# Performance work log

Hardware: AMD Instinct MI355X
Metric: run time of the kernel (lower is better)

Reference implementation:

```python
import jax, jax.numpy as jnp
import numpy as np

N_HEAD = 16
MASK_VALUE = -10000.0


def setup_inputs() -> dict:
    key = jax.random.key(0)
    ks = jax.random.split(key, 5)
    B, S, D = 2, 2048, 1024
    return {
        "x": jax.random.normal(ks[0], (B, S, D), dtype=jnp.float32),
        "qkv_w": jax.random.normal(ks[1], (D, 3 * D), dtype=jnp.float32) * 0.02,
        "qkv_b": jnp.zeros((3 * D,), dtype=jnp.float32),
        "proj_w": jax.random.normal(ks[2], (D, D), dtype=jnp.float32) * 0.02,
        "proj_b": jnp.zeros((D,), dtype=jnp.float32),
    }


def reference(x, qkv_w, qkv_b, proj_w, proj_b):
    B, S, D = x.shape
    H = N_HEAD
    hd = D // H

    # fused QKV projection, then split (torch.split along last dim)
    qkv = x @ qkv_w + qkv_b                      # [B, S, 3D]
    q, k, v = jnp.split(qkv, 3, axis=-1)

    def split_heads(t):  # [B, S, D] -> [B, H, S, hd]
        return t.reshape(B, S, H, hd).transpose(0, 2, 1, 3)

    q, k, v = split_heads(q), split_heads(k), split_heads(v)

    # scaled dot-product scores (scale_attn_weights=True)
    scores = jnp.einsum("bhqd,bhkd->bhqk", q, k) / jnp.sqrt(jnp.asarray(hd, x.dtype))

    # causal mask: tril over [query_len, key_len] (no cache, so q_len == k_len == S)
    causal = jnp.tril(jnp.ones((S, S), dtype=bool))[None, None]
    scores = jnp.where(causal, scores, jnp.asarray(MASK_VALUE, x.dtype))

    attn = jax.nn.softmax(scores, axis=-1)       # dropout p=0 (eval): identity
    out = jnp.einsum("bhqk,bhkd->bhqd", attn, v)

    # merge heads and output projection (resid dropout p=0)
    out = out.transpose(0, 2, 1, 3).reshape(B, S, D)
    out = out @ proj_w + proj_b
    return out
```

## Files before the change

kernel.cpp:

```cpp
#include <hip/hip_runtime.h>
#include <hip/hip_bf16.h>


#define SEQ 2048
#define DM 1024
#define HD 64
#define NHEAD 16
#define BHTOT 32

typedef unsigned short u16;
typedef __bf16 bf16_t;
typedef bf16_t bf16x8 __attribute__((ext_vector_type(8)));
typedef float f32x4 __attribute__((ext_vector_type(4)));
typedef float f32x16 __attribute__((ext_vector_type(16)));

__device__ __forceinline__ u16 f2bf(float f) {
  unsigned u = __float_as_uint(f);
  u += 0x7fffu + ((u >> 16) & 1u);
  return (u16)(u >> 16);
}

__device__ __forceinline__ f32x4 mfma16(uint4 a, uint4 b, f32x4 c) {
  return __builtin_amdgcn_mfma_f32_16x16x32_bf16(
      __builtin_bit_cast(bf16x8, a), __builtin_bit_cast(bf16x8, b), c, 0, 0, 0);
}

__device__ __forceinline__ f32x16 mfma32(uint4 a, uint4 b, f32x16 c) {
  return __builtin_amdgcn_mfma_f32_32x32x16_bf16(
      __builtin_bit_cast(bf16x8, a), __builtin_bit_cast(bf16x8, b), c, 0, 0, 0);
}

__device__ __forceinline__ unsigned cvtpk(float lo, float hi) {
  unsigned d;
  asm("v_cvt_pk_bf16_f32 %0, %1, %2" : "=v"(d) : "v"(lo), "v"(hi));
  return d;
}

__device__ __forceinline__ void gload_lds16(const u16* g, void* l) {
  __builtin_amdgcn_global_load_lds(
      (const __attribute__((address_space(1))) unsigned*)g,
      (__attribute__((address_space(3))) unsigned*)l, 16, 0, 0);
}

__global__ __launch_bounds__(256) void cvt_bf16(const float* __restrict__ in,
                                                u16* __restrict__ out) {
  int i = (blockIdx.x * 256 + threadIdx.x) * 4;
  float4 v = *(const float4*)(in + i);
  uint2 pk;
  pk.x = (unsigned)f2bf(v.x) | ((unsigned)f2bf(v.y) << 16);
  pk.y = (unsigned)f2bf(v.z) | ((unsigned)f2bf(v.w) << 16);
  *(uint2*)(out + i) = pk;
}

__global__ __launch_bounds__(256) void transpose_w(const float* __restrict__ W,
                                                   u16* __restrict__ Wt,
                                                   int K, int N) {
  __shared__ u16 t[32][33];
  const int n0 = blockIdx.x * 32, k0 = blockIdx.y * 32;
  const int tx = threadIdx.x & 31, ty = threadIdx.x >> 5;
#pragma unroll
  for (int i = 0; i < 4; ++i) {
    int k = ty + i * 8;
    t[tx][k] = f2bf(W[(size_t)(k0 + k) * N + n0 + tx]);
  }
  __syncthreads();
#pragma unroll
  for (int i = 0; i < 4; ++i) {
    int n = ty + i * 8;
    Wt[(size_t)(n0 + n) * K + k0 + tx] = t[n][tx];
  }
}

__global__ __launch_bounds__(256) void qkv_gemm(
    const u16* __restrict__ A, const u16* __restrict__ Bt,
    const float* __restrict__ bias,
    u16* __restrict__ qb, u16* __restrict__ kb, u16* __restrict__ vb) {
  __shared__ u16 Al[128 * 32];
  __shared__ u16 Bl[128 * 32];
  const int tid = threadIdx.x;
  const int m0 = blockIdx.y * 128;
  const int n0 = blockIdx.x * 128;
  const int w = tid >> 6, lane = tid & 63;
  const int lr = lane & 15, lg = lane >> 4;
  const int wm = (w >> 1) * 64, wn = (w & 1) * 64;
  const int Kd = DM;

  f32x4 acc[4][4] = {};

  for (int kk = 0; kk < Kd; kk += 32) {
    __syncthreads();
#pragma unroll
    for (int i = 0; i < 2; ++i) {
      int off = (i * 4 + w) * 1024 + lane * 16;
      int row = off >> 6, colb = off & 63;
      gload_lds16(A + (size_t)(m0 + row) * Kd + kk + (colb >> 1),
                  (char*)Al + (i * 4 + w) * 1024);
      gload_lds16(Bt + (size_t)(n0 + row) * Kd + kk + (colb >> 1),
                  (char*)Bl + (i * 4 + w) * 1024);
    }
    __syncthreads();
    uint4 af[4], bfr[4];
#pragma unroll
    for (int mi = 0; mi < 4; ++mi)
      af[mi] = *(const uint4*)(Al + (wm + mi * 16 + lr) * 32 + lg * 8);
#pragma unroll
    for (int ni = 0; ni < 4; ++ni)
      bfr[ni] = *(const uint4*)(Bl + (wn + ni * 16 + lr) * 32 + lg * 8);
#pragma unroll
    for (int mi = 0; mi < 4; ++mi)
#pragma unroll
      for (int ni = 0; ni < 4; ++ni)
        acc[mi][ni] = mfma16(af[mi], bfr[ni], acc[mi][ni]);
  }

#pragma unroll
  for (int mi = 0; mi < 4; ++mi) {
#pragma unroll
    for (int ni = 0; ni < 4; ++ni) {
#pragma unroll
      for (int r = 0; r < 4; ++r) {
        int m = m0 + wm + mi * 16 + lg * 4 + r;
        int n = n0 + wn + ni * 16 + lr;
        float v = acc[mi][ni][r] + bias[n];
        int part = n >> 10;
        int d = n & 1023;
        int h = d >> 6, dim = d & 63;
        int b = m >> 11, s = m & 2047;
        int bh = b * NHEAD + h;
        if (part == 0)
          qb[((size_t)bh * SEQ + s) * HD + dim] = f2bf(v * 0.18033688f);
        else if (part == 1)
          kb[((size_t)bh * SEQ + s) * HD + dim] = f2bf(v);
        else
          vb[((size_t)bh * HD + dim) * SEQ + s] = f2bf(v);
      }
    }
  }
}

__global__ __launch_bounds__(128) void attn_kernel(
    const u16* __restrict__ Q, const u16* __restrict__ K,
    const u16* __restrict__ Vt, u16* __restrict__ O) {
  const int lane = threadIdx.x & 63;
  const int w = threadIdx.x >> 6;
  const int r31 = lane & 31;
  const int hi = lane >> 5;
  const int bh = blockIdx.x & 31;
  const int j = 31 - (blockIdx.x >> 5);
  const int qt = 2 * j + w;
  const int q0w = qt * 32;
  const int nst = j + 1;

  const u16* Qb = Q + (size_t)bh * SEQ * HD;
  const u16* Kb = K + (size_t)bh * SEQ * HD;
  const u16* Vb = Vt + (size_t)bh * HD * SEQ;

  uint4 qf[4];
#pragma unroll
  for (int ks = 0; ks < 4; ++ks)
    qf[ks] = *(const uint4*)(Qb + (size_t)(q0w + r31) * HD + ks * 16 + hi * 8);

  f32x16 ot0 = {}, ot1 = {};
  float L = 0.f;

#define LOADK(KF, kv0)                                                          \
  {                                                                             \
    _Pragma("unroll") for (int ks = 0; ks < 4; ++ks) {                          \
      KF[ks] = *(const uint4*)(Kb + (size_t)((kv0) + r31) * HD + ks * 16 + hi * 8); \
      KF[ks + 4] =                                                              \
          *(const uint4*)(Kb + (size_t)((kv0) + 32 + r31) * HD + ks * 16 + hi * 8); \
    }                                                                           \
  }

#define RELAYOUT(dst, S, base)                                                  \
  {                                                                             \
    unsigned e01 = cvtpk(S[base + 0], S[base + 1]), e23 = cvtpk(S[base + 2], S[base + 3]); \
    unsigned e45 = cvtpk(S[base + 4], S[base + 5]), e67 = cvtpk(S[base + 6], S[base + 7]); \
    unsigned p01 = __shfl_xor(e01, 32), p23 = __shfl_xor(e23, 32);              \
    unsigned p45 = __shfl_xor(e45, 32), p67 = __shfl_xor(e67, 32);              \
    dst.x = hi ? p45 : e01;                                                     \
    dst.y = hi ? p67 : e23;                                                     \
    dst.z = hi ? e45 : p01;                                                     \
    dst.w = hi ? e67 : p23;                                                     \
  }

#define STEP(KF, KN)                                                            \
  {                                                                             \
    const int kv0 = t << 6;                                                     \
    const bool last = (t == nst - 1);                                           \
    const bool skip1 = last && ((qt & 1) == 0);   \
    uint4 vf[8];                                                                \
    _Pragma("unroll") for (int ks = 0; ks < 2; ++ks) {                          \
      vf[ks] = *(const uint4*)(Vb + (size_t)r31 * SEQ + kv0 + ks * 16 + hi * 8); \
      vf[ks + 4] =                                                              \
          *(const uint4*)(Vb + (size_t)(32 + r31) * SEQ + kv0 + ks * 16 + hi * 8); \
    }                                                                           \
    if (!skip1) {                                                               \
      _Pragma("unroll") for (int ks = 2; ks < 4; ++ks) {                        \
        vf[ks] = *(const uint4*)(Vb + (size_t)r31 * SEQ + kv0 + ks * 16 + hi * 8); \
        vf[ks + 4] =                                                            \
            *(const uint4*)(Vb + (size_t)(32 + r31) * SEQ + kv0 + ks * 16 + hi * 8); \
      }                                                                         \
    }                                                                           \
    f32x16 s0 = {}, s1 = {};                                                    \
    _Pragma("unroll") for (int ks = 0; ks < 4; ++ks)                            \
        s0 = mfma32(KF[ks], qf[ks], s0);                                        \
    if (!skip1) {                                                               \
      _Pragma("unroll") for (int ks = 0; ks < 4; ++ks)                          \
          s1 = mfma32(KF[ks + 4], qf[ks], s1);                                  \
    }                                                                           \
    if (t + 1 < nst) LOADK(KN, kv0 + 64);                                       \
    if (last) {                                                                 \
      _Pragma("unroll") for (int i = 0; i < 16; ++i) {                          \
        const int row = (i & 3) + 8 * (i >> 2) + 4 * hi;                        \
        if (skip1) {                                                            \
          if (row > r31) s0[i] = -1e30f;                                        \
        } else {                                                                \
          if (row > r31) s1[i] = -1e30f;                                        \
        }                                                                       \
      }                                                                         \
    }                                                                           \
    float rs = 0.f;                                                             \
    _Pragma("unroll") for (int i = 0; i < 16; ++i) {                            \
      s0[i] = __builtin_exp2f(s0[i]);                                           \
      rs += s0[i];                                                              \
    }                                                                           \
    if (!skip1) {                                                               \
      _Pragma("unroll") for (int i = 0; i < 16; ++i) {                          \
        s1[i] = __builtin_exp2f(s1[i]);                                         \
        rs += s1[i];                                                            \
      }                                                                         \
    }                                                                           \
    L += rs;                                                                    \
    uint4 pa[4];                                                                \
    RELAYOUT(pa[0], s0, 0);                                                     \
    RELAYOUT(pa[1], s0, 8);                                                     \
    if (!skip1) {                                                               \
      RELAYOUT(pa[2], s1, 0);                                                   \
      RELAYOUT(pa[3], s1, 8);                                                   \
    }                                                                           \
    _Pragma("unroll") for (int ks = 0; ks < 2; ++ks) {                          \
      ot0 = mfma32(vf[ks], pa[ks], ot0);                                        \
      ot1 = mfma32(vf[ks + 4], pa[ks], ot1);                                    \
    }                                                                           \
    if (!skip1) {                                                               \
      _Pragma("unroll") for (int ks = 2; ks < 4; ++ks) {                        \
        ot0 = mfma32(vf[ks], pa[ks], ot0);                                      \
        ot1 = mfma32(vf[ks + 4], pa[ks], ot1);                                  \
      }                                                                         \
    }                                                                           \
  }

  uint4 kA[8], kB[8];
  LOADK(kA, 0);
  int t = 0;
  for (;;) {
    STEP(kA, kB);
    if (++t >= nst) break;
    STEP(kB, kA);
    if (++t >= nst) break;
  }
#undef STEP
#undef RELAYOUT
#undef LOADK

  L += __shfl_xor(L, 32);
  const float inv = 1.0f / L;
  const int b = bh >> 4, h = bh & 15;
  u16* Orow = O + ((size_t)b * SEQ + q0w + r31) * DM + h * HD;
#pragma unroll
  for (int g = 0; g < 4; ++g) {
    uint2 p0, p1;
    p0.x = (unsigned)f2bf(ot0[4 * g + 0] * inv) | ((unsigned)f2bf(ot0[4 * g + 1] * inv) << 16);
    p0.y = (unsigned)f2bf(ot0[4 * g + 2] * inv) | ((unsigned)f2bf(ot0[4 * g + 3] * inv) << 16);
    p1.x = (unsigned)f2bf(ot1[4 * g + 0] * inv) | ((unsigned)f2bf(ot1[4 * g + 1] * inv) << 16);
    p1.y = (unsigned)f2bf(ot1[4 * g + 2] * inv) | ((unsigned)f2bf(ot1[4 * g + 3] * inv) << 16);
    *(uint2*)(Orow + 8 * g + 4 * hi) = p0;
    *(uint2*)(Orow + 32 + 8 * g + 4 * hi) = p1;
  }
}

__global__ __launch_bounds__(256) void proj_gemm(
    const u16* __restrict__ A, const u16* __restrict__ Bt,
    const float* __restrict__ bias, float* __restrict__ out) {
  __shared__ u16 Al[128 * 32];
  __shared__ u16 Bl[128 * 32];
  const int tid = threadIdx.x;
  const int m0 = blockIdx.y * 128;
  const int n0 = blockIdx.x * 128;
  const int w = tid >> 6, lane = tid & 63;
  const int lr = lane & 15, lg = lane >> 4;
  const int wm = (w >> 1) * 64, wn = (w & 1) * 64;
  const int Kd = DM;

  f32x4 acc[4][4] = {};

  for (int kk = 0; kk < Kd; kk += 32) {
    __syncthreads();
#pragma unroll
    for (int i = 0; i < 2; ++i) {
      int off = (i * 4 + w) * 1024 + lane * 16;
      int row = off >> 6, colb = off & 63;
      gload_lds16(A + (size_t)(m0 + row) * Kd + kk + (colb >> 1),
                  (char*)Al + (i * 4 + w) * 1024);
      gload_lds16(Bt + (size_t)(n0 + row) * Kd + kk + (colb >> 1),
                  (char*)Bl + (i * 4 + w) * 1024);
    }
    __syncthreads();
    uint4 af[4], bfr[4];
#pragma unroll
    for (int mi = 0; mi < 4; ++mi)
      af[mi] = *(const uint4*)(Al + (wm + mi * 16 + lr) * 32 + lg * 8);
#pragma unroll
    for (int ni = 0; ni < 4; ++ni)
      bfr[ni] = *(const uint4*)(Bl + (wn + ni * 16 + lr) * 32 + lg * 8);
#pragma unroll
    for (int mi = 0; mi < 4; ++mi)
#pragma unroll
      for (int ni = 0; ni < 4; ++ni)
        acc[mi][ni] = mfma16(af[mi], bfr[ni], acc[mi][ni]);
  }

#pragma unroll
  for (int mi = 0; mi < 4; ++mi)
#pragma unroll
    for (int ni = 0; ni < 4; ++ni)
#pragma unroll
      for (int r = 0; r < 4; ++r) {
        int m = m0 + wm + mi * 16 + lg * 4 + r;
        int n = n0 + wn + ni * 16 + lr;
        out[(size_t)m * DM + n] = acc[mi][ni][r] + bias[n];
      }
}

extern "C" void kernel_launch(void* const* d_in, const int* in_sizes, int n_in,
                              void* d_out, int out_size, void* d_ws, size_t ws_size,
                              hipStream_t stream) {
  const float* x      = (const float*)d_in[0];
  const float* qkv_w  = (const float*)d_in[1];
  const float* qkv_b  = (const float*)d_in[2];
  const float* proj_w = (const float*)d_in[3];
  const float* proj_b = (const float*)d_in[4];
  float* out = (float*)d_out;

  const size_t per = (size_t)BHTOT * SEQ * HD;
  u16* qb = (u16*)d_ws;
  u16* kb = qb + per;
  u16* vb = kb + per;
  u16* xb = vb + per;
  u16* ab = xb;
  u16* wqkvT = xb + (size_t)SEQ * 2 * DM;
  u16* wprojT = wqkvT + (size_t)3072 * DM;

  dim3 blk(256);
  cvt_bf16<<<dim3(4096), blk, 0, stream>>>(x, xb);
  transpose_w<<<dim3(96, 32), blk, 0, stream>>>(qkv_w, wqkvT, DM, 3072);
  transpose_w<<<dim3(32, 32), blk, 0, stream>>>(proj_w, wprojT, DM, DM);
  qkv_gemm<<<dim3(24, 32), blk, 0, stream>>>(xb, wqkvT, qkv_b, qb, kb, vb);
  attn_kernel<<<dim3(1024), dim3(128), 0, stream>>>(qb, kb, vb, ab);
  proj_gemm<<<dim3(8, 32), blk, 0, stream>>>(ab, wprojT, proj_b, out);
}
```

Baseline: 146.4 us.

## Software-pipeline QK^T one tile ahead of softmax and PV in attention

Restructures the attention inner loop so the QK^T MFMAs for the next KV tile are issued before the softmax and PV of the current tile, using double-buffered score accumulators. K for tile t+2 is prefetched into the freed buffer. MFMA sections are wrapped in s_setprio to favour matrix issue, and launch bounds request two blocks per CU. The aim is to overlap exp/relayout VALU work with matrix work, at the cost of more register pressure. The next tile's QK^T no longer applies the skip1 shortcut, so it always computes both halves.

After: 180.6 us. +23.4%, slower.

```diff
diff --git a/kernel.cpp b/kernel.cpp
--- a/kernel.cpp
+++ b/kernel.cpp
@@ -138,7 +138,7 @@
   }
 }
 
-__global__ __launch_bounds__(128) void attn_kernel(
+__global__ __launch_bounds__(128, 2) void attn_kernel(
     const u16* __restrict__ Q, const u16* __restrict__ K,
     const u16* __restrict__ Vt, u16* __restrict__ O) {
   const int lane = threadIdx.x & 63;
@@ -184,7 +184,7 @@
     dst.w = hi ? e67 : p23;                                                     \
   }
 
-#define STEP(KF, KN)                                                            \
+#define STEPP(SC0, SC1, SN0, SN1, KC, KN)                                       \
   {                                                                             \
     const int kv0 = t << 6;                                                     \
     const bool last = (t == nst - 1);                                           \
@@ -202,43 +202,48 @@
             *(const uint4*)(Vb + (size_t)(32 + r31) * SEQ + kv0 + ks * 16 + hi * 8); \
       }                                                                         \
     }                                                                           \
-    f32x16 s0 = {}, s1 = {};                                                    \
-    _Pragma("unroll") for (int ks = 0; ks < 4; ++ks)                            \
-        s0 = mfma32(KF[ks], qf[ks], s0);                                        \
-    if (!skip1) {                                                               \
-      _Pragma("unroll") for (int ks = 0; ks < 4; ++ks)                          \
-          s1 = mfma32(KF[ks + 4], qf[ks], s1);                                  \
-    }                                                                           \
-    if (t + 1 < nst) LOADK(KN, kv0 + 64);                                       \
+            \
+    if (!last) {                                                                \
+      SN0 = (f32x16){};                                                         \
+      SN1 = (f32x16){};                                                         \
+      __builtin_amdgcn_s_setprio(1);                                            \
+      _Pragma("unroll") for (int ks = 0; ks < 4; ++ks) {                        \
+        SN0 = mfma32(KN[ks], qf[ks], SN0);                                      \
+        SN1 = mfma32(KN[ks + 4], qf[ks], SN1);                                  \
+      }                                                                         \
+      __builtin_amdgcn_s_setprio(0);                                            \
+    }                                                                           \
+    if (t + 2 < nst) LOADK(KC, (t + 2) << 6);                                   \
     if (last) {                                                                 \
       _Pragma("unroll") for (int i = 0; i < 16; ++i) {                          \
         const int row = (i & 3) + 8 * (i >> 2) + 4 * hi;                        \
         if (skip1) {                                                            \
-          if (row > r31) s0[i] = -1e30f;                                        \
+          if (row > r31) SC0[i] = -1e30f;                                       \
         } else {                                                                \
-          if (row > r31) s1[i] = -1e30f;                                        \
+          if (row > r31) SC1[i] = -1e30f;                                       \
         }                                                                       \
       }                                                                         \
     }                                                                           \
     float rs = 0.f;                                                             \
     _Pragma("unroll") for (int i = 0; i < 16; ++i) {                            \
-      s0[i] = __builtin_exp2f(s0[i]);                                           \
-      rs += s0[i];                                                              \
+      SC0[i] = __builtin_exp2f(SC0[i]);                                         \
+      rs += SC0[i];                                                             \
     }                                                                           \
     if (!skip1) {                                                               \
       _Pragma("unroll") for (int i = 0; i < 16; ++i) {                          \
-        s1[i] = __builtin_exp2f(s1[i]);                                         \
-        rs += s1[i];                                                            \
+        SC1[i] = __builtin_exp2f(SC1[i]);                                       \
+        rs += SC1[i];                                                           \
       }                                                                         \
     }                                                                           \
     L += rs;                                                                    \
     uint4 pa[4];                                                                \
-    RELAYOUT(pa[0], s0, 0);                                                     \
-    RELAYOUT(pa[1], s0, 8);                                                     \
+    RELAYOUT(pa[0], SC0, 0);                                                    \
+    RELAYOUT(pa[1], SC0, 8);                                                    \
     if (!skip1) {                                                               \
-      RELAYOUT(pa[2], s1, 0);                                                   \
-      RELAYOUT(pa[3], s1, 8);                                                   \
-    }                                                                           \
+      RELAYOUT(pa[2], SC1, 0);                                                  \
+      RELAYOUT(pa[3], SC1, 8);                                                  \
+    }                                                                           \
+    __builtin_amdgcn_s_setprio(1);                                              \
     _Pragma("unroll") for (int ks = 0; ks < 2; ++ks) {                          \
       ot0 = mfma32(vf[ks], pa[ks], ot0);                                        \
       ot1 = mfma32(vf[ks + 4], pa[ks], ot1);                                    \
@@ -249,18 +254,29 @@
         ot1 = mfma32(vf[ks + 4], pa[ks], ot1);                                  \
       }                                                                         \
     }                                                                           \
+    __builtin_amdgcn_s_setprio(0);                                              \
   }
 
   uint4 kA[8], kB[8];
+  f32x16 sA0, sA1, sB0, sB1;
   LOADK(kA, 0);
+  LOADK(kB, 64);
+  sA0 = (f32x16){};
+  sA1 = (f32x16){};
+#pragma unroll
+  for (int ks = 0; ks < 4; ++ks) {
+    sA0 = mfma32(kA[ks], qf[ks], sA0);
+    sA1 = mfma32(kA[ks + 4], qf[ks], sA1);
+  }
+
   int t = 0;
   for (;;) {
-    STEP(kA, kB);
+    STEPP(sA0, sA1, sB0, sB1, kA, kB);
     if (++t >= nst) break;
-    STEP(kB, kA);
+    STEPP(sB0, sB1, sA0, sA1, kB, kA);
     if (++t >= nst) break;
   }
-#undef STEP
+#undef STEPP
 #undef RELAYOUT
 #undef LOADK
 
```

## Prefetch V tiles one step ahead and remap blocks to head order

Applied to the files above, without the earlier changes.

The attention kernel now loads the next V tile together with the next K tile right after the QK MFMAs, double-buffering V instead of K, so V loads overlap the softmax and PV work. The K tile is reloaded in place into a single buffer, which relies on the QK MFMAs having consumed it first. The block-to-head mapping is permuted, likely to spread heads across XCDs or cache slices. The exp-sum reduction is split into four partial accumulators to shorten the dependency chain. On the last masked step V is now loaded in full even when half of it is unused.

Result: slower. 162.1 us (+10.7%).

```diff
diff --git a/kernel.cpp b/kernel.cpp
--- a/kernel.cpp
+++ b/kernel.cpp
@@ -145,8 +145,9 @@
   const int w = threadIdx.x >> 6;
   const int r31 = lane & 31;
   const int hi = lane >> 5;
-  const int bh = blockIdx.x & 31;
-  const int j = 31 - (blockIdx.x >> 5);
+  const int bid = blockIdx.x;
+  const int bh = ((bid & 7) << 2) | ((bid >> 3) & 3);
+  const int j = 31 - (bid >> 5);
   const int qt = 2 * j + w;
   const int q0w = qt * 32;
   const int nst = j + 1;
@@ -169,6 +170,15 @@
       KF[ks] = *(const uint4*)(Kb + (size_t)((kv0) + r31) * HD + ks * 16 + hi * 8); \
       KF[ks + 4] =                                                              \
           *(const uint4*)(Kb + (size_t)((kv0) + 32 + r31) * HD + ks * 16 + hi * 8); \
+    }                                                                           \
+  }
+
+#define LOADV(VF, kv0)                                                          \
+  {                                                                             \
+    _Pragma("unroll") for (int ks = 0; ks < 4; ++ks) {                          \
+      VF[ks] = *(const uint4*)(Vb + (size_t)r31 * SEQ + (kv0) + ks * 16 + hi * 8); \
+      VF[ks + 4] =                                                              \
+          *(const uint4*)(Vb + (size_t)(32 + r31) * SEQ + (kv0) + ks * 16 + hi * 8); \
     }                                                                           \
   }
 
@@ -184,32 +194,22 @@
     dst.w = hi ? e67 : p23;                                                     \
   }
 
-#define STEP(KF, KN)                                                            \
+#define STEPP(VF, VN)                                                           \
   {                                                                             \
     const int kv0 = t << 6;                                                     \
     const bool last = (t == nst - 1);                                           \
     const bool skip1 = last && ((qt & 1) == 0);   \
-    uint4 vf[8];                                                                \
-    _Pragma("unroll") for (int ks = 0; ks < 2; ++ks) {                          \
-      vf[ks] = *(const uint4*)(Vb + (size_t)r31 * SEQ + kv0 + ks * 16 + hi * 8); \
-      vf[ks + 4] =                                                              \
-          *(const uint4*)(Vb + (size_t)(32 + r31) * SEQ + kv0 + ks * 16 + hi * 8); \
-    }                                                                           \
-    if (!skip1) {                                                               \
-      _Pragma("unroll") for (int ks = 2; ks < 4; ++ks) {                        \
-        vf[ks] = *(const uint4*)(Vb + (size_t)r31 * SEQ + kv0 + ks * 16 + hi * 8); \
-        vf[ks + 4] =                                                            \
-            *(const uint4*)(Vb + (size_t)(32 + r31) * SEQ + kv0 + ks * 16 + hi * 8); \
-      }                                                                         \
-    }                                                                           \
     f32x16 s0 = {}, s1 = {};                                                    \
     _Pragma("unroll") for (int ks = 0; ks < 4; ++ks)                            \
-        s0 = mfma32(KF[ks], qf[ks], s0);                                        \
+        s0 = mfma32(kf[ks], qf[ks], s0);                                        \
     if (!skip1) {                                                               \
       _Pragma("unroll") for (int ks = 0; ks < 4; ++ks)                          \
-          s1 = mfma32(KF[ks + 4], qf[ks], s1);                                  \
-    }                                                                           \
-    if (t + 1 < nst) LOADK(KN, kv0 + 64);                                       \
+          s1 = mfma32(kf[ks + 4], qf[ks], s1);                                  \
+    }                                                                           \
+    if (t + 1 < nst) {                                                          \
+      LOADK(kf, kv0 + 64);                                                      \
+      LOADV(VN, kv0 + 64);                                                      \
+    }                                                                           \
     if (last) {                                                                 \
       _Pragma("unroll") for (int i = 0; i < 16; ++i) {                          \
         const int row = (i & 3) + 8 * (i >> 2) + 4 * hi;                        \
@@ -220,18 +220,31 @@
         }                                                                       \
       }                                                                         \
     }                                                                           \
-    float rs = 0.f;                                                             \
-    _Pragma("unroll") for (int i = 0; i < 16; ++i) {                            \
-      s0[i] = __builtin_exp2f(s0[i]);                                           \
-      rs += s0[i];                                                              \
+             \
+    float ra = 0.f, rb = 0.f, rc = 0.f, rd = 0.f;                               \
+    _Pragma("unroll") for (int i = 0; i < 4; ++i) {                             \
+      s0[4 * i + 0] = __builtin_exp2f(s0[4 * i + 0]);                           \
+      s0[4 * i + 1] = __builtin_exp2f(s0[4 * i + 1]);                           \
+      s0[4 * i + 2] = __builtin_exp2f(s0[4 * i + 2]);                           \
+      s0[4 * i + 3] = __builtin_exp2f(s0[4 * i + 3]);                           \
+      ra += s0[4 * i + 0];                                                      \
+      rb += s0[4 * i + 1];                                                      \
+      rc += s0[4 * i + 2];                                                      \
+      rd += s0[4 * i + 3];                                                      \
     }                                                                           \
     if (!skip1) {                                                               \
-      _Pragma("unroll") for (int i = 0; i < 16; ++i) {                          \
-        s1[i] = __builtin_exp2f(s1[i]);                                         \
-        rs += s1[i];                                                            \
+      _Pragma("unroll") for (int i = 0; i < 4; ++i) {                           \
+        s1[4 * i + 0] = __builtin_exp2f(s1[4 * i + 0]);                         \
+        s1[4 * i + 1] = __builtin_exp2f(s1[4 * i + 1]);                         \
+        s1[4 * i + 2] = __builtin_exp2f(s1[4 * i + 2]);                         \
+        s1[4 * i + 3] = __builtin_exp2f(s1[4 * i + 3]);                         \
+        ra += s1[4 * i + 0];                                                    \
+        rb += s1[4 * i + 1];                                                    \
+        rc += s1[4 * i + 2];                                                    \
+        rd += s1[4 * i + 3];                                                    \
       }                                                                         \
     }                                                                           \
-    L += rs;                                                                    \
+    L += (ra + rb) + (rc + rd);                                                 \
     uint4 pa[4];                                                                \
     RELAYOUT(pa[0], s0, 0);                                                     \
     RELAYOUT(pa[1], s0, 8);                                                     \
@@ -240,28 +253,30 @@
       RELAYOUT(pa[3], s1, 8);                                                   \
     }                                                                           \
     _Pragma("unroll") for (int ks = 0; ks < 2; ++ks) {                          \
-      ot0 = mfma32(vf[ks], pa[ks], ot0);                                        \
-      ot1 = mfma32(vf[ks + 4], pa[ks], ot1);                                    \
+      ot0 = mfma32(VF[ks], pa[ks], ot0);                                        \
+      ot1 = mfma32(VF[ks + 4], pa[ks], ot1);                                    \
     }                                                                           \
     if (!skip1) {                                                               \
       _Pragma("unroll") for (int ks = 2; ks < 4; ++ks) {                        \
-        ot0 = mfma32(vf[ks], pa[ks], ot0);                                      \
-        ot1 = mfma32(vf[ks + 4], pa[ks], ot1);                                  \
+        ot0 = mfma32(VF[ks], pa[ks], ot0);                                      \
+        ot1 = mfma32(VF[ks + 4], pa[ks], ot1);                                  \
       }                                                                         \
     }                                                                           \
   }
 
-  uint4 kA[8], kB[8];
-  LOADK(kA, 0);
+  uint4 kf[8], vA[8], vB[8];
+  LOADK(kf, 0);
+  LOADV(vA, 0);
   int t = 0;
   for (;;) {
-    STEP(kA, kB);
+    STEPP(vA, vB);
     if (++t >= nst) break;
-    STEP(kB, kA);
+    STEPP(vB, vA);
     if (++t >= nst) break;
   }
-#undef STEP
+#undef STEPP
 #undef RELAYOUT
+#undef LOADV
 #undef LOADK
 
   L += __shfl_xor(L, 32);
```

## Fuse preprocessing kernels into one launch and retile output projection GEMM

Applied to the files above, without the earlier changes.

Merges the input bf16 conversion and both weight transposes into a single prep kernel, removing two launches. The transpose now reads float4 vectors and writes 16-byte packed stores using a 32x128 tile. The projection GEMM switches to 128x64 tiles, which doubles its grid from 256 to 512 blocks so more of the CUs are occupied. In exchange, each block reuses less data per tile and the transpose uses more LDS.

Result: faster. 140.7 us (-3.9%).

```diff
diff --git a/kernel.cpp b/kernel.cpp
--- a/kernel.cpp
+++ b/kernel.cpp
@@ -42,32 +42,60 @@
       (__attribute__((address_space(3))) unsigned*)l, 16, 0, 0);
 }
 
-__global__ __launch_bounds__(256) void cvt_bf16(const float* __restrict__ in,
-                                                u16* __restrict__ out) {
-  int i = (blockIdx.x * 256 + threadIdx.x) * 4;
-  float4 v = *(const float4*)(in + i);
-  uint2 pk;
-  pk.x = (unsigned)f2bf(v.x) | ((unsigned)f2bf(v.y) << 16);
-  pk.y = (unsigned)f2bf(v.z) | ((unsigned)f2bf(v.w) << 16);
-  *(uint2*)(out + i) = pk;
-}
-
-__global__ __launch_bounds__(256) void transpose_w(const float* __restrict__ W,
-                                                   u16* __restrict__ Wt,
-                                                   int K, int N) {
-  __shared__ u16 t[32][33];
-  const int n0 = blockIdx.x * 32, k0 = blockIdx.y * 32;
-  const int tx = threadIdx.x & 31, ty = threadIdx.x >> 5;
+__device__ __forceinline__ void ttile(const float* __restrict__ W,
+                                      u16* __restrict__ Wt, int K, int N,
+                                      int n0, int k0) {
+  __shared__ u16 t[32][132];
+  const int tid = threadIdx.x;
+  const int tx = tid & 31, ty = tid >> 5;
 #pragma unroll
   for (int i = 0; i < 4; ++i) {
-    int k = ty + i * 8;
-    t[tx][k] = f2bf(W[(size_t)(k0 + k) * N + n0 + tx]);
+    const int k = ty + i * 8;
+    float4 v = *(const float4*)(W + (size_t)(k0 + k) * N + n0 + tx * 4);
+    t[k][tx * 4 + 0] = f2bf(v.x);
+    t[k][tx * 4 + 1] = f2bf(v.y);
+    t[k][tx * 4 + 2] = f2bf(v.z);
+    t[k][tx * 4 + 3] = f2bf(v.w);
   }
   __syncthreads();
-#pragma unroll
-  for (int i = 0; i < 4; ++i) {
-    int n = ty + i * 8;
-    Wt[(size_t)(n0 + n) * K + k0 + tx] = t[n][tx];
+  const int n = tid >> 1, half = tid & 1;
+  u16 tmp[16];
+#pragma unroll
+  for (int j = 0; j < 16; ++j) tmp[j] = t[half * 16 + j][n];
+  uint4 lo, hi;
+  lo.x = (unsigned)tmp[0] | ((unsigned)tmp[1] << 16);
+  lo.y = (unsigned)tmp[2] | ((unsigned)tmp[3] << 16);
+  lo.z = (unsigned)tmp[4] | ((unsigned)tmp[5] << 16);
+  lo.w = (unsigned)tmp[6] | ((unsigned)tmp[7] << 16);
+  hi.x = (unsigned)tmp[8] | ((unsigned)tmp[9] << 16);
+  hi.y = (unsigned)tmp[10] | ((unsigned)tmp[11] << 16);
+  hi.z = (unsigned)tmp[12] | ((unsigned)tmp[13] << 16);
+  hi.w = (unsigned)tmp[14] | ((unsigned)tmp[15] << 16);
+  u16* base = Wt + (size_t)(n0 + n) * K + k0 + half * 16;
+  *(uint4*)base = lo;
+  *(uint4*)(base + 8) = hi;
+}
+
+__global__ __launch_bounds__(256) void prep(
+    const float* __restrict__ x, const float* __restrict__ wqkv,
+    const float* __restrict__ wproj, u16* __restrict__ xb,
+    u16* __restrict__ wqkvT, u16* __restrict__ wprojT) {
+  const int bid = blockIdx.x;
+  if (bid < 4096) {
+    int i = (bid * 256 + threadIdx.x) * 4;
+    float4 v = *(const float4*)(x + i);
+    uint2 pk;
+    pk.x = (unsigned)f2bf(v.x) | ((unsigned)f2bf(v.y) << 16);
+    pk.y = (unsigned)f2bf(v.z) | ((unsigned)f2bf(v.w) << 16);
+    *(uint2*)(xb + i) = pk;
+  } else if (bid < 4096 + 768) {
+    const int tb = bid - 4096;
+    const int nt = tb % 24, kt = tb / 24;
+    ttile(wqkv, wqkvT, DM, 3072, nt * 128, kt * 32);
+  } else {
+    const int tb = bid - 4864;
+    const int nt = tb & 7, kt = tb >> 3;
+    ttile(wproj, wprojT, DM, DM, nt * 128, kt * 32);
   }
 }
 
@@ -284,16 +312,16 @@
     const u16* __restrict__ A, const u16* __restrict__ Bt,
     const float* __restrict__ bias, float* __restrict__ out) {
   __shared__ u16 Al[128 * 32];
-  __shared__ u16 Bl[128 * 32];
+  __shared__ u16 Bl[64 * 32];
   const int tid = threadIdx.x;
   const int m0 = blockIdx.y * 128;
-  const int n0 = blockIdx.x * 128;
+  const int n0 = blockIdx.x * 64;
   const int w = tid >> 6, lane = tid & 63;
   const int lr = lane & 15, lg = lane >> 4;
-  const int wm = (w >> 1) * 64, wn = (w & 1) * 64;
+  const int wm = w * 32;
   const int Kd = DM;
 
-  f32x4 acc[4][4] = {};
+  f32x4 acc[2][4] = {};
 
   for (int kk = 0; kk < Kd; kk += 32) {
     __syncthreads();
@@ -303,32 +331,36 @@
       int row = off >> 6, colb = off & 63;
       gload_lds16(A + (size_t)(m0 + row) * Kd + kk + (colb >> 1),
                   (char*)Al + (i * 4 + w) * 1024);
+    }
+    {
+      int off = w * 1024 + lane * 16;
+      int row = off >> 6, colb = off & 63;
       gload_lds16(Bt + (size_t)(n0 + row) * Kd + kk + (colb >> 1),
-                  (char*)Bl + (i * 4 + w) * 1024);
+                  (char*)Bl + w * 1024);
     }
     __syncthreads();
-    uint4 af[4], bfr[4];
-#pragma unroll
-    for (int mi = 0; mi < 4; ++mi)
+    uint4 af[2], bfr[4];
+#pragma unroll
+    for (int mi = 0; mi < 2; ++mi)
       af[mi] = *(const uint4*)(Al + (wm + mi * 16 + lr) * 32 + lg * 8);
 #pragma unroll
     for (int ni = 0; ni < 4; ++ni)
-      bfr[ni] = *(const uint4*)(Bl + (wn + ni * 16 + lr) * 32 + lg * 8);
-#pragma unroll
-    for (int mi = 0; mi < 4; ++mi)
+      bfr[ni] = *(const uint4*)(Bl + (ni * 16 + lr) * 32 + lg * 8);
+#pragma unroll
+    for (int mi = 0; mi < 2; ++mi)
 #pragma unroll
       for (int ni = 0; ni < 4; ++ni)
         acc[mi][ni] = mfma16(af[mi], bfr[ni], acc[mi][ni]);
   }
 
 #pragma unroll
-  for (int mi = 0; mi < 4; ++mi)
+  for (int mi = 0; mi < 2; ++mi)
 #pragma unroll
     for (int ni = 0; ni < 4; ++ni)
 #pragma unroll
       for (int r = 0; r < 4; ++r) {
         int m = m0 + wm + mi * 16 + lg * 4 + r;
-        int n = n0 + wn + ni * 16 + lr;
+        int n = n0 + ni * 16 + lr;
         out[(size_t)m * DM + n] = acc[mi][ni][r] + bias[n];
       }
 }
@@ -353,10 +385,8 @@
   u16* wprojT = wqkvT + (size_t)3072 * DM;
 
   dim3 blk(256);
-  cvt_bf16<<<dim3(4096), blk, 0, stream>>>(x, xb);
-  transpose_w<<<dim3(96, 32), blk, 0, stream>>>(qkv_w, wqkvT, DM, 3072);
-  transpose_w<<<dim3(32, 32), blk, 0, stream>>>(proj_w, wprojT, DM, DM);
+  prep<<<dim3(5120), blk, 0, stream>>>(x, qkv_w, proj_w, xb, wqkvT, wprojT);
   qkv_gemm<<<dim3(24, 32), blk, 0, stream>>>(xb, wqkvT, qkv_b, qb, kb, vb);
   attn_kernel<<<dim3(1024), dim3(128), 0, stream>>>(qb, kb, vb, ab);
-  proj_gemm<<<dim3(8, 32), blk, 0, stream>>>(ab, wprojT, proj_b, out);
-}
+  proj_gemm<<<dim3(16, 32), blk, 0, stream>>>(ab, wprojT, proj_b, out);
+}
```
